# Performance work log

Measured on AMD Instinct MI355X. Metric: run time of the kernel, lower is better.

## Reference

```python
import jax, jax.numpy as jnp
import numpy as np
import math

B, N, D, H, HC = 2, 2048, 1024, 16, 8
HIDDEN = 4 * D
MAX_PERIOD = 10000.0


def _timestep_embedding(t, dim):
    half = dim // 2
    freqs = jnp.exp(-math.log(MAX_PERIOD) * jnp.arange(half, dtype=jnp.float32) / half)
    args = t[:, None] * freqs[None, :]
    return jnp.concatenate([jnp.cos(args), jnp.sin(args)], axis=-1)


def _layer_norm(x, scale, bias, eps=1e-6):
    mu = jnp.mean(x, axis=-1, keepdims=True)
    var = jnp.mean(jnp.square(x - mu), axis=-1, keepdims=True)
    return (x - mu) * jax.lax.rsqrt(var + eps) * scale + bias


def _modulate(x, shift, scale):
    return x * (1.0 + scale[:, None, :]) + shift[:, None, :]


def setup_inputs():
    key = jax.random.key(0)
    ks = jax.random.split(key, 16)

    def dense(k, fin, fout):
        return jax.random.normal(k, (fin, fout), dtype=jnp.float32) / np.sqrt(fin)

    return {
        'x': jax.random.normal(ks[0], (B, N, D), dtype=jnp.float32),
        't': jax.random.uniform(ks[1], (B,), dtype=jnp.float32) * 1000.0,
        'norm1_scale': jnp.ones((D,), jnp.float32),
        'norm1_bias': jnp.zeros((D,), jnp.float32),
        'norm2_scale': jnp.ones((D,), jnp.float32),
        'norm2_bias': jnp.zeros((D,), jnp.float32),
        'tc_w1': dense(ks[2], HIDDEN, HIDDEN),
        'tc_b1': jnp.zeros((HIDDEN,), jnp.float32),
        'tc_w2': dense(ks[3], HIDDEN, HIDDEN),
        'tc_b2': jnp.zeros((HIDDEN,), jnp.float32),
        'tc_wa': 0.02 * dense(ks[4], HIDDEN, 4 * D),
        'tc_ba': jnp.zeros((4 * D,), jnp.float32),
        'tc_wc': 0.02 * dense(ks[5], HIDDEN, 4 * D),
        'tc_bc': jnp.zeros((4 * D,), jnp.float32),
        'attn_qk_w': dense(ks[6], D, D),
        'attn_v_w': dense(ks[7], D, D),
        'attn_out_w': dense(ks[8], D, D),
        'doob_w': 0.02 * dense(ks[9], D, 1),
        'doob_b': jnp.zeros((1,), jnp.float32),
        'ch_qk_w': dense(ks[10], D, D),
        'ch_v_w': dense(ks[11], D, D),
        'ch_out_w': dense(ks[12], D, D),
        'tau': jnp.ones((HC, 1, 1), jnp.float32),
        'gamma1': 1e-4 * jnp.ones((D,), jnp.float32),
        'gamma2': 1e-4 * jnp.ones((D,), jnp.float32),
    }


def reference(x, t, norm1_scale, norm1_bias, norm2_scale, norm2_bias,
              tc_w1, tc_b1, tc_w2, tc_b2, tc_wa, tc_ba, tc_wc, tc_bc,
              attn_qk_w, attn_v_w, attn_out_w, doob_w, doob_b,
              ch_qk_w, ch_v_w, ch_out_w, tau, gamma1, gamma2):
    # ---- AdaLN time conditioning ----
    emb = _timestep_embedding(t, HIDDEN)                 # (B, HIDDEN)
    h = jax.nn.silu(emb @ tc_w1 + tc_b1)
    h = jax.nn.silu(h @ tc_w2 + tc_b2)
    a_shift, a_scale, a_gate, a_lg = jnp.split(h @ tc_wa + tc_ba, 4, axis=-1)
    c_shift, c_scale, c_gate, c_lg = jnp.split(h @ tc_wc + tc_bc, 4, axis=-1)

    # ---- token-diffusion attention (MHDM, tied Q=K, Doob tilt) ----
    x1 = _modulate(_layer_norm(x, norm1_scale, norm1_bias), a_shift, a_scale)
    qk = (x1 @ attn_qk_w) * jnp.exp(a_lg)[:, None, :]    # (B,N,D)
    v = x1 @ attn_v_w
    dh = D // H
    qh = qk.reshape(B, N, H, dh).transpose(0, 2, 1, 3)   # (B,H,N,dh)
    vh = v.reshape(B, N, H, dh).transpose(0, 2, 1, 3)
    dot = jnp.einsum('bhmd,bhnd->bhmn', qh, qh)
    q2 = jnp.sum(qh * qh, axis=-1)
    logits = 2.0 * dot - q2[:, :, :, None] - q2[:, :, None, :]
    phi = (x1 @ doob_w + doob_b)[..., 0]                 # (B,N) destination tilt
    logits = logits + phi[:, None, None, :]
    attn = jax.nn.softmax(logits, axis=-1)
    w = jnp.einsum('bhmn,bhnd->bhmd', attn, vh)
    attn_out = w.transpose(0, 2, 1, 3).reshape(B, N, D) @ attn_out_w
    x = x + attn_out * a_gate[:, None, :] * gamma1

    # ---- channel-diffusion attention ----
    x2 = _modulate(_layer_norm(x, norm2_scale, norm2_bias), c_shift, c_scale)
    qkc = (x2 @ ch_qk_w) * jnp.exp(c_lg)[:, None, :]
    vc = x2 @ ch_v_w
    dhc = D // HC
    qkc = qkc.transpose(0, 2, 1).reshape(B, HC, dhc, N)  # (B,HC,dhc,N)
    vc = vc.transpose(0, 2, 1).reshape(B, HC, dhc, N)
    dotc = jnp.einsum('bhcn,bhdn->bhcd', qkc, qkc)
    q2c = jnp.sum(qkc * qkc, axis=-1)                    # (B,HC,dhc)
    logitsc = (2.0 * dotc - q2c[:, :, :, None] - q2c[:, :, None, :]) / math.sqrt(N)
    logitsc = logitsc * tau[None, ...]
    attnc = jax.nn.softmax(logitsc, axis=-1)
    wc = jnp.einsum('bhcd,bhdn->bhcn', attnc, vc)
    ch_out = wc.reshape(B, D, N).transpose(0, 2, 1) @ ch_out_w
    x = x + ch_out * c_gate[:, None, :] * gamma2
    return x
```

## Files before the change

kernel.cpp:

```cpp
#include <hip/hip_runtime.h>
#include <hip/hip_bf16.h>
#include <math.h>

typedef __bf16 bf16;
typedef bf16 bf16x8 __attribute__((ext_vector_type(8)));
typedef bf16 bf16x4 __attribute__((ext_vector_type(4)));
typedef bf16 bf16x2 __attribute__((ext_vector_type(2)));
typedef float f32x4 __attribute__((ext_vector_type(4)));

#define B_   2
#define N_   2048
#define D_   1024
#define H_   16
#define HC_  8
#define M_   (B_*N_)

__device__ __forceinline__ void gl16(const bf16* g, bf16* lds_base) {
#if __has_builtin(__builtin_amdgcn_global_load_lds)
  __builtin_amdgcn_global_load_lds((const __attribute__((address_space(1))) void*)g,
                                   (__attribute__((address_space(3))) void*)lds_base,
                                   16, 0, 0);
#else
  int lane = threadIdx.x & 63;
  *(uint4*)(lds_base + lane * 8) = *(const uint4*)g;
#endif
}

__device__ __forceinline__ void gl4(const float* g, float* lds_base) {
#if __has_builtin(__builtin_amdgcn_global_load_lds)
  __builtin_amdgcn_global_load_lds((const __attribute__((address_space(1))) void*)g,
                                   (__attribute__((address_space(3))) void*)lds_base,
                                   4, 0, 0);
#else
  int lane = threadIdx.x & 63;
  lds_base[lane] = *g;
#endif
}

__device__ __forceinline__ bf16x2 cvt_pk_bf16(float lo, float hi) {
  unsigned int r;
  asm("v_cvt_pk_bf16_f32 %0, %1, %2" : "=v"(r) : "v"(lo), "v"(hi));
  union { unsigned int u; bf16x2 v; } c;
  c.u = r;
  return c.v;
}

__device__ __forceinline__ int vperm(int kv) {
  return (((kv >> 4) & 1) << 5) | (((kv >> 2) & 3) << 3) | (((kv >> 5) & 1) << 2) | (kv & 3);
}

__global__ __launch_bounds__(256) void emb_kernel(const float* __restrict__ tin,
                                                  float* __restrict__ emb) {
  int idx = blockIdx.x * 256 + threadIdx.x;
  int b = idx >> 12, p = idx & 4095;
  float tv = tin[b];
  int half = p & 2047;
  float freq = expf(-logf(10000.f) * (float)half * (1.f / 2048.f));
  float arg = tv * freq;
  emb[idx] = (p < 2048) ? cosf(arg) : sinf(arg);
}

__global__ __launch_bounds__(256) void gemv_kernel(const float* __restrict__ x,
                                                   const float* __restrict__ W,
                                                   float* __restrict__ part) {
  __shared__ float xs[2][128];
  int t = threadIdx.x;
  int j0 = blockIdx.x * 512;
  int k0 = blockIdx.y * 128;
  if (t < 128) xs[0][t] = x[k0 + t];
  else         xs[1][t - 128] = x[4096 + k0 + (t - 128)];
  __syncthreads();
  float a00 = 0.f, a01 = 0.f, a10 = 0.f, a11 = 0.f;
  int j = j0 + t * 2;
  #pragma unroll 8
  for (int k = 0; k < 128; k++) {
    float2 wv = *(const float2*)(W + (size_t)(k0 + k) * 4096 + j);
    float x0 = xs[0][k], x1 = xs[1][k];
    a00 += x0 * wv.x; a01 += x0 * wv.y;
    a10 += x1 * wv.x; a11 += x1 * wv.y;
  }
  *(float2*)(part + (size_t)(blockIdx.y * 2 + 0) * 4096 + j) = make_float2(a00, a01);
  *(float2*)(part + (size_t)(blockIdx.y * 2 + 1) * 4096 + j) = make_float2(a10, a11);
}

__global__ __launch_bounds__(256) void gemv_reduce_kernel(const float* __restrict__ part,
                                                          const float* __restrict__ bias,
                                                          float* __restrict__ y, int act) {
  int idx = blockIdx.x * 256 + threadIdx.x;
  int b = idx >> 12, j = idx & 4095;
  float s = bias[j];
  #pragma unroll
  for (int kc = 0; kc < 32; kc++) s += part[(size_t)(kc * 2 + b) * 4096 + j];
  if (act) s = s / (1.f + expf(-s));
  y[idx] = s;
}

__global__ __launch_bounds__(256) void postA_kernel(const float* __restrict__ avec,
                                                    const float* __restrict__ cvec,
                                                    const float* __restrict__ g1,
                                                    const float* __restrict__ g2,
                                                    float* __restrict__ sca, float* __restrict__ scc,
                                                    float* __restrict__ agv, float* __restrict__ cgv) {
  int idx = blockIdx.x * 256 + threadIdx.x;
  int b = idx >> 10, d = idx & 1023;
  sca[idx] = expf(avec[b * 4096 + 3072 + d]);
  scc[idx] = expf(cvec[b * 4096 + 3072 + d]);
  agv[idx] = avec[b * 4096 + 2048 + d] * g1[d];
  cgv[idx] = cvec[b * 4096 + 2048 + d] * g2[d];
}

__global__ __launch_bounds__(256) void wtconv6_kernel(const float* w0, const float* w1,
                                                      const float* w2, const float* w3,
                                                      const float* w4, const float* w5,
                                                      bf16* o0, bf16* o1, bf16* o2,
                                                      bf16* o3, bf16* o4, bf16* o5) {
  const float* W; bf16* Wt;
  switch (blockIdx.z) {
    case 0: W = w0; Wt = o0; break;
    case 1: W = w1; Wt = o1; break;
    case 2: W = w2; Wt = o2; break;
    case 3: W = w3; Wt = o3; break;
    case 4: W = w4; Wt = o4; break;
    default: W = w5; Wt = o5; break;
  }
  __shared__ float tile[32][33];
  int t = threadIdx.x;
  int i = t >> 5, j = t & 31;
  int n0 = blockIdx.x * 32, k0 = blockIdx.y * 32;
  #pragma unroll
  for (int u = 0; u < 4; u++) {
    int k = i + u * 8;
    tile[k][j] = W[(size_t)(k0 + k) * 1024 + n0 + j];
  }
  __syncthreads();
  #pragma unroll
  for (int u = 0; u < 4; u++) {
    int n = i + u * 8;
    Wt[(size_t)(n0 + n) * 1024 + k0 + j] = (bf16)tile[j][n];
  }
}

__global__ __launch_bounds__(256) void ln_mod_kernel(const float* __restrict__ xin,
                                                     const float* __restrict__ nsc,
                                                     const float* __restrict__ nbi,
                                                     const float* __restrict__ mod,
                                                     const float* __restrict__ doobw,
                                                     float* __restrict__ phi,
                                                     bf16* __restrict__ outp) {
  int row = blockIdx.x;
  int b = row >> 11;
  int t = threadIdx.x;
  const float* xr = xin + (size_t)row * 1024;
  float v[4], s = 0.f, ss = 0.f;
  #pragma unroll
  for (int u = 0; u < 4; u++) { v[u] = xr[t + u * 256]; s += v[u]; ss += v[u] * v[u]; }
  #pragma unroll
  for (int off = 1; off < 64; off <<= 1) { s += __shfl_xor(s, off, 64); ss += __shfl_xor(ss, off, 64); }
  __shared__ float sb[4], ssb[4], pb[4];
  if ((t & 63) == 0) { sb[t >> 6] = s; ssb[t >> 6] = ss; }
  __syncthreads();
  s = sb[0] + sb[1] + sb[2] + sb[3];
  ss = ssb[0] + ssb[1] + ssb[2] + ssb[3];
  float mu = s * (1.f / 1024.f);
  float var = ss * (1.f / 1024.f) - mu * mu;
  float rs = rsqrtf(var + 1e-6f);
  const float* shv = mod + b * 4096;
  const float* scv = mod + b * 4096 + 1024;
  float ph = 0.f;
  #pragma unroll
  for (int u = 0; u < 4; u++) {
    int d = t + u * 256;
    float y = (v[u] - mu) * rs * nsc[d] + nbi[d];
    float ym = y * (1.f + scv[d]) + shv[d];
    outp[(size_t)row * 1024 + d] = (bf16)ym;
    if (doobw) ph += ym * doobw[d];
  }
  if (doobw) {
    #pragma unroll
    for (int off = 1; off < 64; off <<= 1) ph += __shfl_xor(ph, off, 64);
    if ((t & 63) == 0) pb[t >> 6] = ph;
    __syncthreads();
    if (t == 0) phi[row] = pb[0] + pb[1] + pb[2] + pb[3];
  }
}

__global__ __launch_bounds__(256) void phimax_kernel(const float* __restrict__ phi,
                                                     float* __restrict__ pm) {
  int b = blockIdx.x;
  int t = threadIdx.x;
  float m = -1e30f;
  #pragma unroll
  for (int u = 0; u < 8; u++) m = fmaxf(m, phi[b * 2048 + t + u * 256]);
  #pragma unroll
  for (int off = 1; off < 64; off <<= 1) m = fmaxf(m, __shfl_xor(m, off, 64));
  __shared__ float mb[4];
  if ((t & 63) == 0) mb[t >> 6] = m;
  __syncthreads();
  if (t == 0) pm[b] = fmaxf(fmaxf(mb[0], mb[1]), fmaxf(mb[2], mb[3]));
}

template <int MODE, int TM>
__global__ __launch_bounds__(256) void gemm_kernel(const bf16* __restrict__ A,
                                                   const bf16* __restrict__ Wt,
                                                   const float* __restrict__ scale,
                                                   const float* __restrict__ resid,
                                                   void* __restrict__ out0,
                                                   void* __restrict__ out1) {
  constexpr int K = 1024;
  constexpr int WM = TM / 2;
  constexpr int IT = WM / 16;
  __shared__ bf16 As[TM * 64];
  __shared__ bf16 Bs[128 * 64];
  const int m0 = blockIdx.x * TM;
  const int n0 = blockIdx.y * 128;
  const int t = threadIdx.x, lane = t & 63, wid = t >> 6;
  const int wy = wid >> 1, wx = wid & 1;
  const int ml = lane & 15, quad = lane >> 4, rq = quad * 4, kq = quad * 8;
  const int srow = lane >> 3;
  const int schunk = (lane & 7) ^ srow;
  const bf16* gA = A  + (size_t)(m0 + wid * (TM / 4) + srow) * K + schunk * 8;
  const bf16* gB = Wt + (size_t)(n0 + wid * 32 + srow) * K + schunk * 8;
  bf16* lA = As + (wid * (TM / 4)) * 64;
  bf16* lB = Bs + (wid * 32) * 64;
  const int mlm = ml & 7;

  f32x4 acc[IT][4] = {};
  for (int k0 = 0; k0 < K; k0 += 64) {
    __syncthreads();
    #pragma unroll
    for (int q = 0; q < TM / 32; q++)
      gl16(gA + (size_t)q * 8 * K + k0, lA + q * 8 * 64);
    #pragma unroll
    for (int q = 0; q < 4; q++)
      gl16(gB + (size_t)q * 8 * K + k0, lB + q * 8 * 64);
    __syncthreads();
    #pragma unroll
    for (int ks = 0; ks < 2; ks++) {
      const int slot = ((ks * 4 + quad) ^ mlm) * 8;
      bf16x8 af[IT], bfv[4];
      #pragma unroll
      for (int i = 0; i < IT; i++)
        af[i] = *(const bf16x8*)(As + (wy * WM + i * 16 + ml) * 64 + slot);
      #pragma unroll
      for (int j = 0; j < 4; j++)
        bfv[j] = *(const bf16x8*)(Bs + (wx * 64 + j * 16 + ml) * 64 + slot);
      #pragma unroll
      for (int i = 0; i < IT; i++)
        #pragma unroll
        for (int j = 0; j < 4; j++)
          acc[i][j] = __builtin_amdgcn_mfma_f32_16x16x32_bf16(af[i], bfv[j], acc[i][j], 0, 0, 0);
    }
  }
  #pragma unroll
  for (int i = 0; i < IT; i++) {
    #pragma unroll
    for (int j = 0; j < 4; j++) {
      int col = n0 + wx * 64 + j * 16 + ml;
      int row0 = m0 + wy * WM + i * 16 + rq;
      int b0 = row0 >> 11, nn0 = row0 & 2047;
      if constexpr (MODE == 10) {
        if (col < 1024) {
          int h = col >> 6, dh = col & 63;
          float sv = scale[b0 * 1024 + col];
          #pragma unroll
          for (int r = 0; r < 4; r++)
            ((bf16*)out0)[((size_t)(b0 * 16 + h) * 2048 + nn0 + r) * 64 + dh] =
                (bf16)(acc[i][j][r] * sv);
        } else {
          int c2 = col - 1024;
          int h = c2 >> 6, dh = c2 & 63;
          int c = vperm(nn0 & 63);
          union { bf16x4 v; bf16x2 h2[2]; } pk;
          pk.h2[0] = cvt_pk_bf16(acc[i][j][0], acc[i][j][1]);
          pk.h2[1] = cvt_pk_bf16(acc[i][j][2], acc[i][j][3]);
          *(bf16x4*)((bf16*)out1 +
              (((size_t)(b0 * 16 + h) * 32 + (nn0 >> 6)) * 64 + dh) * 64 + c) = pk.v;
        }
      } else if constexpr (MODE == 11) {
        if (col < 1024) {
          float sv = scale[b0 * 1024 + col];
          union { bf16x4 v; bf16x2 h2[2]; } pk;
          pk.h2[0] = cvt_pk_bf16(acc[i][j][0] * sv, acc[i][j][1] * sv);
          pk.h2[1] = cvt_pk_bf16(acc[i][j][2] * sv, acc[i][j][3] * sv);
          *(bf16x4*)((bf16*)out0 +
              ((size_t)((b0 * 8 + (col >> 7)) * 128 + (col & 127))) * 2048 + nn0) = pk.v;
        } else {
          #pragma unroll
          for (int r = 0; r < 4; r++)
            ((bf16*)out1)[(size_t)(row0 + r) * 1024 + (col - 1024)] = (bf16)acc[i][j][r];
        }
      } else {
        float g = scale[b0 * 1024 + col];
        #pragma unroll
        for (int r = 0; r < 4; r++)
          ((float*)out0)[(size_t)(row0 + r) * 1024 + col] =
              resid[(size_t)(row0 + r) * 1024 + col] + acc[i][j][r] * g;
      }
    }
  }
}

__global__ __launch_bounds__(256) void q2e_kernel(const bf16* __restrict__ qkh,
                                                  const float* __restrict__ phi,
                                                  const float* __restrict__ pm,
                                                  float* __restrict__ q2buf,
                                                  float* __restrict__ ebuf) {
  int idx = blockIdx.x * 256 + threadIdx.x;
  int bh = idx >> 11, n = idx & 2047;
  int b = bh >> 4;
  const bf16* qr = qkh + (size_t)idx * 64;
  float q = 0.f;
  #pragma unroll
  for (int u = 0; u < 8; u++) {
    bf16x8 v = *(const bf16x8*)(qr + u * 8);
    #pragma unroll
    for (int e = 0; e < 8; e++) { float f = (float)v[e]; q += f * f; }
  }
  q2buf[idx] = q * 1.44269504f;
  ebuf[idx]  = (phi[b * 2048 + n] - q - pm[b]) * 1.44269504f;
}

__global__ __launch_bounds__(256, 4) void flash_kernel(const bf16* __restrict__ qkh,
                                                       const bf16* __restrict__ vtb,
                                                       const float* __restrict__ q2buf,
                                                       const float* __restrict__ ebuf,
                                                       bf16* __restrict__ wout) {
  int bid = blockIdx.x;
  int ii = bid >> 3;
  int bh = (bid & 7) * 4 + (ii >> 5);
  int mt = ii & 31;
  int b = bh >> 4, h = bh & 15;
  int m0 = mt * 64;
  int t = threadIdx.x, lane = t & 63, w = t >> 6;
  int ml = lane & 15, quad = lane >> 4;
  int mlm = ml & 7;

  __shared__ __align__(16) bf16 Ks[2][64 * 64];
  __shared__ __align__(16) bf16 Vs[2][64 * 64];
  __shared__ __align__(16) float Es[2][64];

  int sr = lane >> 3, swz = (lane & 7) ^ sr;
  const bf16* gK = qkh + ((size_t)bh * 2048 + w * 16 + sr) * 64 + swz * 8;
  const bf16* gV = vtb + (size_t)bh * 131072 + (w * 16 + sr) * 64 + swz * 8;
  const float* ep = ebuf + (size_t)bh * 2048;

  const bf16* qrow = qkh + ((size_t)bh * 2048 + m0 + w * 16 + ml) * 64;
  bf16x8 qf0 = *(const bf16x8*)(qrow + quad * 8);
  bf16x8 qf1 = *(const bf16x8*)(qrow + 32 + quad * 8);

  float q2l = q2buf[(size_t)bh * 2048 + m0 + w * 16 + ml];

  f32x4 oacc[4] = {};
  float rs = 0.f;

  gl16(gK,       &Ks[0][w * 1024]);
  gl16(gK + 512, &Ks[0][w * 1024 + 512]);
  gl16(gV,       &Vs[0][w * 1024]);
  gl16(gV + 512, &Vs[0][w * 1024 + 512]);
  if (w == 0) gl4(ep + lane, Es[0]);

  #pragma unroll 2
  for (int nc = 0; nc < 32; nc++) {
    int cur = nc & 1;
    __syncthreads();
    if (nc + 1 < 32) {
      const bf16* nk = gK + (size_t)(nc + 1) * 4096;
      const bf16* nv = gV + (size_t)(nc + 1) * 4096;
      bf16* dk = &Ks[cur ^ 1][w * 1024];
      bf16* dv = &Vs[cur ^ 1][w * 1024];
      gl16(nk,       dk);
      gl16(nk + 512, dk + 512);
      gl16(nv,       dv);
      gl16(nv + 512, dv + 512);
      if (w == 0) gl4(ep + (nc + 1) * 64 + lane, Es[cur ^ 1]);
    }
    const bf16* Kc = Ks[cur];
    const bf16* Vc = Vs[cur];

    f32x4 sacc[4] = {};
    __builtin_amdgcn_s_setprio(1);
    #pragma unroll
    for (int ks = 0; ks < 2; ks++) {
      bf16x8 qb = ks ? qf1 : qf0;
      #pragma unroll
      for (int j = 0; j < 4; j++) {
        bf16x8 ka = *(const bf16x8*)(Kc + (j * 16 + ml) * 64 + ((4 * ks + quad) ^ mlm) * 8);
        sacc[j] = __builtin_amdgcn_mfma_f32_16x16x32_bf16(ka, qb, sacc[j], 0, 0, 0);
      }
    }
    __builtin_amdgcn_s_setprio(0);

    float pv[4][4];
    #pragma unroll
    for (int j = 0; j < 4; j++) {
      float4 ev = *(const float4*)(&Es[cur][j * 16 + quad * 4]);
      pv[j][0] = exp2f(fmaf(2.88539008f, sacc[j][0], ev.x - q2l));
      pv[j][1] = exp2f(fmaf(2.88539008f, sacc[j][1], ev.y - q2l));
      pv[j][2] = exp2f(fmaf(2.88539008f, sacc[j][2], ev.z - q2l));
      pv[j][3] = exp2f(fmaf(2.88539008f, sacc[j][3], ev.w - q2l));
      rs += (pv[j][0] + pv[j][1]) + (pv[j][2] + pv[j][3]);
    }
    union { bf16x8 v; bf16x2 h2[4]; } pa0, pa1;
    pa0.h2[0] = cvt_pk_bf16(pv[0][0], pv[0][1]);
    pa0.h2[1] = cvt_pk_bf16(pv[0][2], pv[0][3]);
    pa0.h2[2] = cvt_pk_bf16(pv[2][0], pv[2][1]);
    pa0.h2[3] = cvt_pk_bf16(pv[2][2], pv[2][3]);
    pa1.h2[0] = cvt_pk_bf16(pv[1][0], pv[1][1]);
    pa1.h2[1] = cvt_pk_bf16(pv[1][2], pv[1][3]);
    pa1.h2[2] = cvt_pk_bf16(pv[3][0], pv[3][1]);
    pa1.h2[3] = cvt_pk_bf16(pv[3][2], pv[3][3]);

    __builtin_amdgcn_s_setprio(1);
    #pragma unroll
    for (int ks = 0; ks < 2; ks++) {
      bf16x8 pa = ks ? pa1.v : pa0.v;
      #pragma unroll
      for (int jd = 0; jd < 4; jd++) {
        bf16x8 vb = *(const bf16x8*)(Vc + (jd * 16 + ml) * 64 + ((4 * ks + quad) ^ mlm) * 8);
        oacc[jd] = __builtin_amdgcn_mfma_f32_16x16x32_bf16(pa, vb, oacc[jd], 0, 0, 0);
      }
    }
    __builtin_amdgcn_s_setprio(0);
  }

  rs += __shfl_xor(rs, 16, 64);
  rs += __shfl_xor(rs, 32, 64);
  float rinv = 1.f / rs;

  int rq = quad * 4;
  float rv[4];
  #pragma unroll
  for (int r = 0; r < 4; r++) rv[r] = __shfl(rinv, rq + r, 64);

  bf16* wrow = wout + (size_t)(b * 2048 + m0 + w * 16) * 1024 + h * 64;
  #pragma unroll
  for (int jd = 0; jd < 4; jd++)
    #pragma unroll
    for (int r = 0; r < 4; r++)
      wrow[(size_t)(rq + r) * 1024 + jd * 16 + ml] = (bf16)(oacc[jd][r] * rv[r]);
}

__global__ __launch_bounds__(256) void gram_kernel(const bf16* __restrict__ qkct,
                                                   float* __restrict__ dotp) {
  int bh = blockIdx.x, ksl = blockIdx.y;
  const bf16* Q = qkct + (size_t)bh * 128 * 2048 + ksl * 256;
  __shared__ bf16 Ts[128 * 40];
  int t = threadIdx.x, lane = t & 63, w = t >> 6;
  int ml = lane & 15, kq = (lane >> 4) * 8, rq = (lane >> 4) * 4;
  f32x4 acc[2][8] = {};
  for (int k0 = 0; k0 < 256; k0 += 32) {
    __syncthreads();
    #pragma unroll
    for (int u = 0; u < 2; u++) {
      int idx = u * 256 + t;
      int r = idx >> 2, seg = (idx & 3) * 8;
      *(uint4*)(Ts + r * 40 + seg) = *(const uint4*)(Q + (size_t)r * 2048 + k0 + seg);
    }
    __syncthreads();
    bf16x8 afr[2], bfr[8];
    #pragma unroll
    for (int i = 0; i < 2; i++) afr[i] = *(const bf16x8*)(Ts + (w * 32 + i * 16 + ml) * 40 + kq);
    #pragma unroll
    for (int j = 0; j < 8; j++) bfr[j] = *(const bf16x8*)(Ts + (j * 16 + ml) * 40 + kq);
    #pragma unroll
    for (int i = 0; i < 2; i++)
      #pragma unroll
      for (int j = 0; j < 8; j++)
        acc[i][j] = __builtin_amdgcn_mfma_f32_16x16x32_bf16(afr[i], bfr[j], acc[i][j], 0, 0, 0);
  }
  float* outp = dotp + ((size_t)ksl * 16 + bh) * 16384;
  #pragma unroll
  for (int i = 0; i < 2; i++)
    #pragma unroll
    for (int j = 0; j < 8; j++)
      #pragma unroll
      for (int r = 0; r < 4; r++) {
        int c = w * 32 + i * 16 + rq + r, d = j * 16 + ml;
        outp[c * 128 + d] = acc[i][j][r];
      }
}

__global__ __launch_bounds__(128) void chsm_kernel(const float* __restrict__ dotp,
                                                   const float* __restrict__ tau,
                                                   bf16* __restrict__ attnc) {
  int blk = blockIdx.x;
  int bh = blk >> 7, c = blk & 127, hc = bh & 7;
  int d = threadIdx.x;
  float dot = 0.f, dd = 0.f;
  #pragma unroll
  for (int kc = 0; kc < 8; kc++) {
    const float* pp = dotp + ((size_t)kc * 16 + bh) * 16384;
    dot += pp[c * 128 + d];
    dd  += pp[d * 128 + d];
  }
  __shared__ float diag[128];
  __shared__ float red[2], red2[2];
  diag[d] = dd;
  __syncthreads();
  float qc = diag[c];
  float sc = tau[hc] * rsqrtf(2048.f);
  float lg = sc * (2.f * dot - qc - dd);
  float mx = lg;
  #pragma unroll
  for (int off = 1; off < 64; off <<= 1) mx = fmaxf(mx, __shfl_xor(mx, off, 64));
  if ((d & 63) == 0) red[d >> 6] = mx;
  __syncthreads();
  mx = fmaxf(red[0], red[1]);
  float e = exp2f((lg - mx) * 1.44269504f);
  float sm = e;
  #pragma unroll
  for (int off = 1; off < 64; off <<= 1) sm += __shfl_xor(sm, off, 64);
  if ((d & 63) == 0) red2[d >> 6] = sm;
  __syncthreads();
  sm = red2[0] + red2[1];
  attnc[(size_t)bh * 16384 + c * 128 + d] = (bf16)(e / sm);
}

__global__ __launch_bounds__(256) void chav_kernel(const bf16* __restrict__ attnc,
                                                   const bf16* __restrict__ vc,
                                                   bf16* __restrict__ wcn) {
  int nb = blockIdx.x, bh = blockIdx.y;
  int b = bh >> 3, hc = bh & 7;
  int n0 = nb * 64;
  __shared__ bf16 As[128 * 136];
  __shared__ bf16 Bs[64 * 136];
  int t = threadIdx.x, lane = t & 63, w = t >> 6;
  int ml = lane & 15, kq = (lane >> 4) * 8, rq = (lane >> 4) * 4;
  #pragma unroll
  for (int u = 0; u < 8; u++) {
    int idx = u * 256 + t;
    int r = idx >> 4, seg = (idx & 15) * 8;
    *(uint4*)(As + r * 136 + seg) = *(const uint4*)(attnc + (size_t)bh * 16384 + r * 128 + seg);
  }
  #pragma unroll
  for (int u = 0; u < 4; u++) {
    int idx = u * 256 + t;
    int r = idx >> 4, seg = (idx & 15) * 8;
    *(uint4*)(Bs + r * 136 + seg) =
        *(const uint4*)(vc + (size_t)(b * 2048 + n0 + r) * 1024 + hc * 128 + seg);
  }
  __syncthreads();
  f32x4 acc[2][4] = {};
  #pragma unroll
  for (int ks = 0; ks < 4; ks++) {
    bf16x8 afr[2], bfr[4];
    #pragma unroll
    for (int i = 0; i < 2; i++)
      afr[i] = *(const bf16x8*)(As + (w * 32 + i * 16 + ml) * 136 + ks * 32 + kq);
    #pragma unroll
    for (int j = 0; j < 4; j++)
      bfr[j] = *(const bf16x8*)(Bs + (j * 16 + ml) * 136 + ks * 32 + kq);
    #pragma unroll
    for (int i = 0; i < 2; i++)
      #pragma unroll
      for (int j = 0; j < 4; j++)
        acc[i][j] = __builtin_amdgcn_mfma_f32_16x16x32_bf16(afr[i], bfr[j], acc[i][j], 0, 0, 0);
  }
  #pragma unroll
  for (int i = 0; i < 2; i++)
    #pragma unroll
    for (int j = 0; j < 4; j++)
      #pragma unroll
      for (int r = 0; r < 4; r++) {
        int c = w * 32 + i * 16 + rq + r;
        int n = n0 + j * 16 + ml;
        wcn[(size_t)(b * 2048 + n) * 1024 + hc * 128 + c] = (bf16)acc[i][j][r];
      }
}

extern "C" void kernel_launch(void* const* d_in, const int* in_sizes, int n_in,
                              void* d_out, int out_size, void* d_ws, size_t ws_size,
                              hipStream_t stream) {
  const float* x      = (const float*)d_in[0];
  const float* t      = (const float*)d_in[1];
  const float* n1s    = (const float*)d_in[2];
  const float* n1b    = (const float*)d_in[3];
  const float* n2s    = (const float*)d_in[4];
  const float* n2b    = (const float*)d_in[5];
  const float* tc_w1  = (const float*)d_in[6];
  const float* tc_b1  = (const float*)d_in[7];
  const float* tc_w2  = (const float*)d_in[8];
  const float* tc_b2  = (const float*)d_in[9];
  const float* tc_wa  = (const float*)d_in[10];
  const float* tc_ba  = (const float*)d_in[11];
  const float* tc_wc  = (const float*)d_in[12];
  const float* tc_bc  = (const float*)d_in[13];
  const float* aqk_w  = (const float*)d_in[14];
  const float* av_w   = (const float*)d_in[15];
  const float* aout_w = (const float*)d_in[16];
  const float* doobw  = (const float*)d_in[17];
  const float* cqk_w  = (const float*)d_in[19];
  const float* cv_w   = (const float*)d_in[20];
  const float* cout_w = (const float*)d_in[21];
  const float* tau    = (const float*)d_in[22];
  const float* g1     = (const float*)d_in[23];
  const float* g2     = (const float*)d_in[24];
  float* out = (float*)d_out;

  char* p = (char*)d_ws;
  auto alloc = [&](size_t bytes) -> void* {
    void* r = (void*)p;
    p += (bytes + 255) & ~(size_t)255;
    return r;
  };
  float* emb   = (float*)alloc(2 * 4096 * 4);
  float* partA = (float*)alloc(32 * 2 * 4096 * 4);
  float* partB = (float*)alloc(32 * 2 * 4096 * 4);
  float* h1    = (float*)alloc(2 * 4096 * 4);
  float* h2    = (float*)alloc(2 * 4096 * 4);
  float* avec  = (float*)alloc(2 * 4096 * 4);
  float* cvec  = (float*)alloc(2 * 4096 * 4);
  float* sca   = (float*)alloc(2 * 1024 * 4);
  float* scc   = (float*)alloc(2 * 1024 * 4);
  float* agv   = (float*)alloc(2 * 1024 * 4);
  float* cgv   = (float*)alloc(2 * 1024 * 4);
  float* phi   = (float*)alloc(4096 * 4);
  float* pmax  = (float*)alloc(2 * 4);
  float* q2buf = (float*)alloc(2 * 16 * 2048 * 4);
  float* ebuf  = (float*)alloc(2 * 16 * 2048 * 4);
  float* dotp  = (float*)alloc((size_t)8 * 16 * 16384 * 4);
  bf16* attnc  = (bf16*)alloc(16 * 128 * 128 * 2);
  bf16* wt     = (bf16*)alloc((size_t)6 * 1024 * 1024 * 2);
  bf16* xbf    = (bf16*)alloc((size_t)M_ * 1024 * 2);
  bf16* qkbf   = (bf16*)alloc((size_t)M_ * 1024 * 2);
  bf16* vbuf   = (bf16*)alloc((size_t)M_ * 1024 * 2);
  bf16* wbuf   = (bf16*)alloc((size_t)M_ * 1024 * 2);
  (void)ws_size; (void)in_sizes; (void)n_in; (void)out_size;

  bf16* wt_tok  = wt;
  bf16* wt_out  = wt + (size_t)2 * 1048576;
  bf16* wt_ch   = wt + (size_t)3 * 1048576;
  bf16* wt_cout = wt + (size_t)5 * 1048576;

  dim3 blk(256);
  wtconv6_kernel<<<dim3(32, 32, 6), blk, 0, stream>>>(
      aqk_w, av_w, aout_w, cqk_w, cv_w, cout_w,
      wt_tok, wt_tok + (size_t)1048576, wt_out,
      wt_ch,  wt_ch  + (size_t)1048576, wt_cout);

  emb_kernel<<<32, blk, 0, stream>>>(t, emb);
  gemv_kernel<<<dim3(8, 32), blk, 0, stream>>>(emb, tc_w1, partA);
  gemv_reduce_kernel<<<32, blk, 0, stream>>>(partA, tc_b1, h1, 1);
  gemv_kernel<<<dim3(8, 32), blk, 0, stream>>>(h1, tc_w2, partA);
  gemv_reduce_kernel<<<32, blk, 0, stream>>>(partA, tc_b2, h2, 1);
  gemv_kernel<<<dim3(8, 32), blk, 0, stream>>>(h2, tc_wa, partA);
  gemv_kernel<<<dim3(8, 32), blk, 0, stream>>>(h2, tc_wc, partB);
  gemv_reduce_kernel<<<32, blk, 0, stream>>>(partA, tc_ba, avec, 0);
  gemv_reduce_kernel<<<32, blk, 0, stream>>>(partB, tc_bc, cvec, 0);
  postA_kernel<<<8, blk, 0, stream>>>(avec, cvec, g1, g2, sca, scc, agv, cgv);

  ln_mod_kernel<<<4096, blk, 0, stream>>>(x, n1s, n1b, avec, doobw, phi, xbf);
  phimax_kernel<<<2, blk, 0, stream>>>(phi, pmax);
  gemm_kernel<10, 128><<<dim3(32, 16), blk, 0, stream>>>(xbf, wt_tok, sca, nullptr, qkbf, vbuf);
  q2e_kernel<<<256, blk, 0, stream>>>(qkbf, phi, pmax, q2buf, ebuf);
  flash_kernel<<<dim3(1024), dim3(256), 0, stream>>>(qkbf, vbuf, q2buf, ebuf, wbuf);
  gemm_kernel<4, 64><<<dim3(64, 8), blk, 0, stream>>>(wbuf, wt_out, agv, x, out, nullptr);

  ln_mod_kernel<<<4096, blk, 0, stream>>>(out, n2s, n2b, cvec, nullptr, nullptr, xbf);
  gemm_kernel<11, 128><<<dim3(32, 16), blk, 0, stream>>>(xbf, wt_ch, scc, nullptr, qkbf, vbuf);
  gram_kernel<<<dim3(16, 8), blk, 0, stream>>>(qkbf, dotp);
  chsm_kernel<<<2048, dim3(128), 0, stream>>>(dotp, tau, attnc);
  chav_kernel<<<dim3(32, 16), blk, 0, stream>>>(attnc, vbuf, wbuf);
  gemm_kernel<4, 64><<<dim3(64, 8), blk, 0, stream>>>(wbuf, wt_cout, cgv, out, out, nullptr);
}
```

Before: 544.2 us.

## Triple-buffer K/V/E tiles in flash kernel with vmcnt-based waits

Replaces the double-buffered K/V/E staging in the flash attention kernel with a three-deep ring. The loop is manually unrolled by three and uses explicit s_waitcnt vmcnt(5) plus a raw barrier instead of __syncthreads, so each wave waits only for the oldest in-flight tile. This keeps two tile loads in flight while computing, hiding global-to-LDS latency. In exchange it needs 50% more LDS per block, drops the occupancy hint from 4 to 3 blocks per CU, and now has every wave issue the E-vector load redundantly.

```diff
diff --git a/kernel.cpp b/kernel.cpp
--- a/kernel.cpp
+++ b/kernel.cpp
@@ -320,7 +320,7 @@
   ebuf[idx]  = (phi[b * 2048 + n] - q - pm[b]) * 1.44269504f;
 }
 
-__global__ __launch_bounds__(256, 4) void flash_kernel(const bf16* __restrict__ qkh,
+__global__ __launch_bounds__(256, 3) void flash_kernel(const bf16* __restrict__ qkh,
                                                        const bf16* __restrict__ vtb,
                                                        const float* __restrict__ q2buf,
                                                        const float* __restrict__ ebuf,
@@ -335,15 +335,27 @@
   int ml = lane & 15, quad = lane >> 4;
   int mlm = ml & 7;
 
-  __shared__ __align__(16) bf16 Ks[2][64 * 64];
-  __shared__ __align__(16) bf16 Vs[2][64 * 64];
-  __shared__ __align__(16) float Es[2][64];
+  __shared__ __align__(16) bf16 Ks[3][64 * 64];
+  __shared__ __align__(16) bf16 Vs[3][64 * 64];
+  __shared__ __align__(16) float Es[3][64];
 
   int sr = lane >> 3, swz = (lane & 7) ^ sr;
   const bf16* gK = qkh + ((size_t)bh * 2048 + w * 16 + sr) * 64 + swz * 8;
   const bf16* gV = vtb + (size_t)bh * 131072 + (w * 16 + sr) * 64 + swz * 8;
   const float* ep = ebuf + (size_t)bh * 2048;
 
+  auto stage = [&](int nc, int buf) {
+    const bf16* nk = gK + (size_t)nc * 4096;
+    const bf16* nv = gV + (size_t)nc * 4096;
+    bf16* dk = &Ks[buf][w * 1024];
+    bf16* dv = &Vs[buf][w * 1024];
+    gl16(nk,       dk);
+    gl16(nk + 512, dk + 512);
+    gl16(nv,       dv);
+    gl16(nv + 512, dv + 512);
+    gl4(ep + nc * 64 + lane, Es[buf]);
+  };
+
   const bf16* qrow = qkh + ((size_t)bh * 2048 + m0 + w * 16 + ml) * 64;
   bf16x8 qf0 = *(const bf16x8*)(qrow + quad * 8);
   bf16x8 qf1 = *(const bf16x8*)(qrow + 32 + quad * 8);
@@ -353,30 +365,7 @@
   f32x4 oacc[4] = {};
   float rs = 0.f;
 
-  gl16(gK,       &Ks[0][w * 1024]);
-  gl16(gK + 512, &Ks[0][w * 1024 + 512]);
-  gl16(gV,       &Vs[0][w * 1024]);
-  gl16(gV + 512, &Vs[0][w * 1024 + 512]);
-  if (w == 0) gl4(ep + lane, Es[0]);
-
-  #pragma unroll 2
-  for (int nc = 0; nc < 32; nc++) {
-    int cur = nc & 1;
-    __syncthreads();
-    if (nc + 1 < 32) {
-      const bf16* nk = gK + (size_t)(nc + 1) * 4096;
-      const bf16* nv = gV + (size_t)(nc + 1) * 4096;
-      bf16* dk = &Ks[cur ^ 1][w * 1024];
-      bf16* dv = &Vs[cur ^ 1][w * 1024];
-      gl16(nk,       dk);
-      gl16(nk + 512, dk + 512);
-      gl16(nv,       dv);
-      gl16(nv + 512, dv + 512);
-      if (w == 0) gl4(ep + (nc + 1) * 64 + lane, Es[cur ^ 1]);
-    }
-    const bf16* Kc = Ks[cur];
-    const bf16* Vc = Vs[cur];
-
+  auto compute = [&](const bf16* Kc, const bf16* Vc, const float* Ec) {
     f32x4 sacc[4] = {};
     __builtin_amdgcn_s_setprio(1);
     #pragma unroll
@@ -393,7 +382,7 @@
     float pv[4][4];
     #pragma unroll
     for (int j = 0; j < 4; j++) {
-      float4 ev = *(const float4*)(&Es[cur][j * 16 + quad * 4]);
+      float4 ev = *(const float4*)(&Ec[j * 16 + quad * 4]);
       pv[j][0] = exp2f(fmaf(2.88539008f, sacc[j][0], ev.x - q2l));
       pv[j][1] = exp2f(fmaf(2.88539008f, sacc[j][1], ev.y - q2l));
       pv[j][2] = exp2f(fmaf(2.88539008f, sacc[j][2], ev.z - q2l));
@@ -421,7 +410,36 @@
       }
     }
     __builtin_amdgcn_s_setprio(0);
-  }
+  };
+
+  stage(0, 0);
+  stage(1, 1);
+
+  for (int k3 = 0; k3 < 30; k3 += 3) {
+    asm volatile("s_waitcnt vmcnt(5)" ::: "memory");
+    __builtin_amdgcn_s_barrier();
+    __builtin_amdgcn_sched_barrier(0);
+    stage(k3 + 2, 2);
+    compute(Ks[0], Vs[0], Es[0]);
+    asm volatile("s_waitcnt vmcnt(5)" ::: "memory");
+    __builtin_amdgcn_s_barrier();
+    __builtin_amdgcn_sched_barrier(0);
+    stage(k3 + 3, 0);
+    compute(Ks[1], Vs[1], Es[1]);
+    asm volatile("s_waitcnt vmcnt(5)" ::: "memory");
+    __builtin_amdgcn_s_barrier();
+    __builtin_amdgcn_sched_barrier(0);
+    stage(k3 + 4, 1);
+    compute(Ks[2], Vs[2], Es[2]);
+  }
+  asm volatile("s_waitcnt vmcnt(5)" ::: "memory");
+  __builtin_amdgcn_s_barrier();
+  __builtin_amdgcn_sched_barrier(0);
+  compute(Ks[0], Vs[0], Es[0]);
+  asm volatile("s_waitcnt vmcnt(0)" ::: "memory");
+  __builtin_amdgcn_s_barrier();
+  __builtin_amdgcn_sched_barrier(0);
+  compute(Ks[1], Vs[1], Es[1]);
 
   rs += __shfl_xor(rs, 16, 64);
   rs += __shfl_xor(rs, 32, 64);
```

Result: slower. 559.8 us (+2.9%).
